# Kernel tuning notes

Hardware: AMD Instinct MI355X
Metric: run time of the kernel (lower is better)

## Reference

```python
import jax, jax.numpy as jnp
import numpy as np
import math

B, H, N, D = 4, 8, 2048, 64


def setup_inputs() -> dict:
    key = jax.random.key(0)
    kq, kk, kv = jax.random.split(key, 3)
    q = jax.random.normal(kq, (B, H, N, D), dtype=jnp.float32)
    k = jax.random.normal(kk, (B, H, N, D), dtype=jnp.float32)
    v = jax.random.normal(kv, (B, H, N, D), dtype=jnp.float32)
    return {"q": q, "k": k, "v": v}


def reference(q, k, v):
    # global_attention_Sub: expanded squared L2 distance ||q_i - k_j||^2
    # = qq_i - 2 q_i.k_j + kk_j, then softmax(-dist/sqrt(D)) @ v.
    scale = math.sqrt(q.shape[-1])
    inner = -2.0 * jnp.einsum('bhnd,bhmd->bhnm', q, k)          # [B,H,N,N]
    qq = jnp.sum(q * q, axis=-1, keepdims=True)                  # [B,H,N,1]
    kk = jnp.sum(k * k, axis=-1, keepdims=True)                  # [B,H,N,1]
    diff_sq = qq + inner + jnp.swapaxes(kk, -1, -2)              # [B,H,N,N]
    attn = jax.nn.softmax(-diff_sq / scale, axis=-1)
    x = jnp.einsum('bhnm,bhmd->bhnd', attn, v)                   # [B,H,N,D]
    return jnp.transpose(x, (0, 2, 1, 3))                        # [B,N,H,D]
```

## Files before the change

### kernel.cpp

```cpp
#include <hip/hip_runtime.h>

typedef __bf16 bf16x4 __attribute__((ext_vector_type(4)));
typedef __bf16 bf16x8 __attribute__((ext_vector_type(8)));
typedef float floatx4 __attribute__((ext_vector_type(4)));

constexpr int Bc = 4, Hc = 8, Nc = 2048, Dc = 64;
constexpr int BQ = 128;
constexpr int WQ = 32;
constexpr int TK = 64;
constexpr int NT = Nc / TK;
constexpr int SPS = 72;
constexpr float LOG2E = 1.44269504088896340736f;

constexpr size_t KSW_OFF = 0;
constexpr size_t VSW_OFF = (size_t)32 * NT * 8192;
constexpr size_t KKN_OFF = VSW_OFF * 2;

typedef __attribute__((address_space(1))) const unsigned int gu32;
typedef __attribute__((address_space(3))) unsigned int lu32;
__device__ __forceinline__ void dma16(const void* g, void* l) {
    __builtin_amdgcn_global_load_lds((gu32*)g, (lu32*)l, 16, 0, 0);
}
__device__ __forceinline__ void dma4(const void* g, void* l) {
    __builtin_amdgcn_global_load_lds((gu32*)g, (lu32*)l, 4, 0, 0);
}

__global__ __launch_bounds__(256) void prep_kernel(
    const float* __restrict__ Kg, const float* __restrict__ Vg, char* __restrict__ ws)
{
    __shared__ float sT[64 * 68];
    const int tid = threadIdx.x;
    const int jt = blockIdx.x, bh = blockIdx.y;

    __bf16* Ksw = (__bf16*)(ws + KSW_OFF) + ((size_t)bh * NT + jt) * 4096;
    __bf16* Vsw = (__bf16*)(ws + VSW_OFF) + ((size_t)bh * NT + jt) * 4096;
    float*  kkn = (float*)(ws + KKN_OFF) + (size_t)bh * Nc + jt * 64;
    const size_t tb = ((size_t)bh * Nc + jt * 64) * Dc;

#pragma unroll
    for (int cc = 0; cc < 2; ++cc) {
        const int g   = tid + cc * 256;
        const int key = g >> 3, kcx = g & 7;
        const int kc  = kcx ^ (key & 7);
        const float* src = Kg + tb + key * 64 + kc * 8;
        float4 a = *(const float4*)src;
        float4 b = *(const float4*)(src + 4);
        float ss = a.x*a.x + a.y*a.y + a.z*a.z + a.w*a.w
                 + b.x*b.x + b.y*b.y + b.z*b.z + b.w*b.w;
        ss += __shfl_xor(ss, 1);
        ss += __shfl_xor(ss, 2);
        ss += __shfl_xor(ss, 4);
        if (kcx == 0) kkn[key] = -(ss * 0.125f * LOG2E);
        bf16x8 c8;
        c8[0]=(__bf16)a.x; c8[1]=(__bf16)a.y; c8[2]=(__bf16)a.z; c8[3]=(__bf16)a.w;
        c8[4]=(__bf16)b.x; c8[5]=(__bf16)b.y; c8[6]=(__bf16)b.z; c8[7]=(__bf16)b.w;
        *(bf16x8*)(Ksw + g * 8) = c8;
    }

    {
        const int js = tid >> 2, dc = (tid & 3) * 16;
        const float* vr = Vg + tb + js * 64 + dc;
        float* dst = &sT[js * 68 + dc];
        *(float4*)dst       = *(const float4*)vr;
        *(float4*)(dst + 4) = *(const float4*)(vr + 4);
        *(float4*)(dst + 8) = *(const float4*)(vr + 8);
        *(float4*)(dst + 12)= *(const float4*)(vr + 12);
    }
    __syncthreads();

#pragma unroll
    for (int cc = 0; cc < 2; ++cc) {
        const int g = tid + cc * 256;
        const int d = g >> 3, kcx = g & 7;
        const int kc = kcx ^ (d & 7);
        bf16x8 c8;
#pragma unroll
        for (int e = 0; e < 8; ++e) {
            const int ee = (e + kcx) & 7;
            c8[ee] = (__bf16)sT[(kc * 8 + ee) * 68 + d];
        }
        *(bf16x8*)(Vsw + g * 8) = c8;
    }
}

__global__ __launch_bounds__(256, 2) void attn_kernel(
    const float* __restrict__ Qg, const char* __restrict__ ws, float* __restrict__ Og)
{
    __shared__ __align__(16) __bf16 sK[2][4096];
    __shared__ __align__(16) __bf16 sV[2][4096];
    __shared__ __align__(16) float  skk[2][64];
    __shared__ __align__(16) __bf16 sP[BQ * SPS];
    __shared__ __align__(16) float  sl[BQ];

    const int tid  = threadIdx.x;
    const int wave = tid >> 6;
    const int lane = tid & 63;
    const int qd   = lane >> 4;
    const int c    = lane & 15;

    const int qt = blockIdx.x;
    const int bh = blockIdx.y;

    const char* Kimg = ws + KSW_OFF + (size_t)bh * NT * 8192;
    const char* Vimg = ws + VSW_OFF + (size_t)bh * NT * 8192;
    const float* kkp = (const float*)(ws + KKN_OFF) + (size_t)bh * Nc;

    const float qscale = 0.25f * LOG2E;
    const int i0 = qt * BQ + wave * WQ;

    bf16x8 qf[2][2];
#pragma unroll
    for (int h = 0; h < 2; ++h) {
        const float* qrow = Qg + ((size_t)bh * Nc + i0 + h * 16 + c) * Dc + qd * 8;
#pragma unroll
        for (int ks = 0; ks < 2; ++ks) {
            float4 a = *(const float4*)(qrow + ks * 32);
            float4 b = *(const float4*)(qrow + ks * 32 + 4);
            bf16x8 f;
            f[0] = (__bf16)(a.x * qscale); f[1] = (__bf16)(a.y * qscale);
            f[2] = (__bf16)(a.z * qscale); f[3] = (__bf16)(a.w * qscale);
            f[4] = (__bf16)(b.x * qscale); f[5] = (__bf16)(b.y * qscale);
            f[6] = (__bf16)(b.z * qscale); f[7] = (__bf16)(b.w * qscale);
            qf[h][ks] = f;
        }
    }

    const int koff0 = c * 64 + ((qd ^ (c & 7)) << 3);
    const int koff1 = c * 64 + (((4 + qd) ^ (c & 7)) << 3);

    floatx4 oacc[2][4];
#pragma unroll
    for (int h = 0; h < 2; ++h)
#pragma unroll
        for (int dt = 0; dt < 4; ++dt)
#pragma unroll
            for (int e = 0; e < 4; ++e) oacc[h][dt][e] = 0.f;
    float lp[2] = {0.f, 0.f};

    auto stage = [&](int jt2, int b) {
        const char* ki = Kimg + (size_t)jt2 * 8192;
        const char* vi = Vimg + (size_t)jt2 * 8192;
#pragma unroll
        for (int i = 0; i < 2; ++i) {
            const int off    = wave * 2048 + i * 1024 + lane * 16;
            const int ldsoff = wave * 2048 + i * 1024;
            dma16(ki + off, (char*)&sK[b][0] + ldsoff);
            dma16(vi + off, (char*)&sV[b][0] + ldsoff);
        }
        if (wave == 3) dma4(kkp + jt2 * 64 + lane, &skk[b][0]);
    };

    stage(0, 0);

    for (int jt = 0; jt < NT; ++jt) {
        const int b = jt & 1;
        __syncthreads();
        if (jt + 1 < NT) stage(jt + 1, b ^ 1);

        floatx4 st[2][4];
#pragma unroll
        for (int kt = 0; kt < 4; ++kt) {
            floatx4 kkf = *(const floatx4*)&skk[b][kt * 16 + qd * 4];
            st[0][kt] = kkf; st[1][kt] = kkf;
        }
#pragma unroll
        for (int kt = 0; kt < 4; ++kt) {
            const __bf16* kbase = &sK[b][kt * 1024];
            bf16x8 kf0 = *(const bf16x8*)(kbase + koff0);
            bf16x8 kf1 = *(const bf16x8*)(kbase + koff1);
            st[0][kt] = __builtin_amdgcn_mfma_f32_16x16x32_bf16(kf0, qf[0][0], st[0][kt], 0, 0, 0);
            st[0][kt] = __builtin_amdgcn_mfma_f32_16x16x32_bf16(kf1, qf[0][1], st[0][kt], 0, 0, 0);
            st[1][kt] = __builtin_amdgcn_mfma_f32_16x16x32_bf16(kf0, qf[1][0], st[1][kt], 0, 0, 0);
            st[1][kt] = __builtin_amdgcn_mfma_f32_16x16x32_bf16(kf1, qf[1][1], st[1][kt], 0, 0, 0);
        }

#pragma unroll
        for (int h = 0; h < 2; ++h) {
            const int prow = wave * WQ + h * 16 + c;
#pragma unroll
            for (int kt = 0; kt < 4; ++kt) {
                float p0 = __builtin_amdgcn_exp2f(st[h][kt][0]);
                float p1 = __builtin_amdgcn_exp2f(st[h][kt][1]);
                float p2 = __builtin_amdgcn_exp2f(st[h][kt][2]);
                float p3 = __builtin_amdgcn_exp2f(st[h][kt][3]);
                lp[h] += (p0 + p1) + (p2 + p3);
                bf16x4 pk;
                pk[0] = (__bf16)p0; pk[1] = (__bf16)p1;
                pk[2] = (__bf16)p2; pk[3] = (__bf16)p3;
                *(bf16x4*)&sP[prow * SPS + kt * 16 + qd * 4] = pk;
            }
        }
        bf16x8 pf[2][2];
#pragma unroll
        for (int h = 0; h < 2; ++h)
#pragma unroll
            for (int ks = 0; ks < 2; ++ks)
                pf[h][ks] = *(const bf16x8*)&sP[(wave * WQ + h * 16 + c) * SPS + ks * 32 + qd * 8];

#pragma unroll
        for (int dt = 0; dt < 4; ++dt) {
            const __bf16* vbase = &sV[b][dt * 1024];
            bf16x8 vf0 = *(const bf16x8*)(vbase + koff0);
            bf16x8 vf1 = *(const bf16x8*)(vbase + koff1);
            oacc[0][dt] = __builtin_amdgcn_mfma_f32_16x16x32_bf16(pf[0][0], vf0, oacc[0][dt], 0, 0, 0);
            oacc[0][dt] = __builtin_amdgcn_mfma_f32_16x16x32_bf16(pf[0][1], vf1, oacc[0][dt], 0, 0, 0);
            oacc[1][dt] = __builtin_amdgcn_mfma_f32_16x16x32_bf16(pf[1][0], vf0, oacc[1][dt], 0, 0, 0);
            oacc[1][dt] = __builtin_amdgcn_mfma_f32_16x16x32_bf16(pf[1][1], vf1, oacc[1][dt], 0, 0, 0);
        }
    }

#pragma unroll
    for (int h = 0; h < 2; ++h) {
        float l = lp[h];
        l += __shfl_xor(l, 16);
        l += __shfl_xor(l, 32);
        if (qd == 0) sl[wave * WQ + h * 16 + c] = l;
    }
    const int b_ = bh >> 3, hh = bh & 7;
#pragma unroll
    for (int h = 0; h < 2; ++h) {
        floatx4 lf = *(const floatx4*)&sl[wave * WQ + h * 16 + qd * 4];
#pragma unroll
        for (int r = 0; r < 4; ++r) {
            const float inv = 1.f / lf[r];
            const int i = i0 + h * 16 + qd * 4 + r;
            float* orow = Og + (((size_t)b_ * Nc + i) * Hc + hh) * Dc + c;
#pragma unroll
            for (int dt = 0; dt < 4; ++dt)
                orow[dt * 16] = oacc[h][dt][r] * inv;
        }
    }
}

extern "C" void kernel_launch(void* const* d_in, const int* in_sizes, int n_in,
                              void* d_out, int out_size, void* d_ws, size_t ws_size,
                              hipStream_t stream) {
    const float* q = (const float*)d_in[0];
    const float* k = (const float*)d_in[1];
    const float* v = (const float*)d_in[2];
    float* out = (float*)d_out;
    char* ws = (char*)d_ws;
    prep_kernel<<<dim3(NT, Bc * Hc), 256, 0, stream>>>(k, v, ws);
    attn_kernel<<<dim3(Nc / BQ, Bc * Hc), 256, 0, stream>>>(q, ws, out);
}
```

Before: 140.8 us.

## Software-pipeline PV MMA one tile behind QK to overlap exp with MFMA

Restructures the attention loop so the P·V matrix multiply for the previous key tile runs right after the current tile's QK^T MFMAs, before the exp2 softmax step. This lets the exp/convert work overlap with independent MFMA work instead of being serialised. V staging moves to a triple buffer so the previous tile's V stays resident while the next one is loaded, and the final tile's PV is done after the loop. It costs extra LDS for the third V buffer and extra registers for the carried P fragments, which may lower occupancy.

Result: faster. 137.2 us (-2.5%).

```diff
diff --git a/kernel.cpp b/kernel.cpp
--- a/kernel.cpp
+++ b/kernel.cpp
@@ -56,7 +56,6 @@
         c8[4]=(__bf16)b.x; c8[5]=(__bf16)b.y; c8[6]=(__bf16)b.z; c8[7]=(__bf16)b.w;
         *(bf16x8*)(Ksw + g * 8) = c8;
     }
-
     {
         const int js = tid >> 2, dc = (tid & 3) * 16;
         const float* vr = Vg + tb + js * 64 + dc;
@@ -67,7 +66,6 @@
         *(float4*)(dst + 12)= *(const float4*)(vr + 12);
     }
     __syncthreads();
-
 #pragma unroll
     for (int cc = 0; cc < 2; ++cc) {
         const int g = tid + cc * 256;
@@ -87,7 +85,7 @@
     const float* __restrict__ Qg, const char* __restrict__ ws, float* __restrict__ Og)
 {
     __shared__ __align__(16) __bf16 sK[2][4096];
-    __shared__ __align__(16) __bf16 sV[2][4096];
+    __shared__ __align__(16) __bf16 sVall[3 * 4096];
     __shared__ __align__(16) float  skk[2][64];
     __shared__ __align__(16) __bf16 sP[BQ * SPS];
     __shared__ __align__(16) float  sl[BQ];
@@ -137,25 +135,31 @@
             for (int e = 0; e < 4; ++e) oacc[h][dt][e] = 0.f;
     float lp[2] = {0.f, 0.f};
 
-    auto stage = [&](int jt2, int b) {
+    __bf16* vprev = &sVall[2 * 4096];
+    __bf16* vcur  = &sVall[0];
+    __bf16* vnext = &sVall[1 * 4096];
+
+    auto stage = [&](int jt2, int kb, __bf16* vdst) {
         const char* ki = Kimg + (size_t)jt2 * 8192;
         const char* vi = Vimg + (size_t)jt2 * 8192;
 #pragma unroll
         for (int i = 0; i < 2; ++i) {
             const int off    = wave * 2048 + i * 1024 + lane * 16;
             const int ldsoff = wave * 2048 + i * 1024;
-            dma16(ki + off, (char*)&sK[b][0] + ldsoff);
-            dma16(vi + off, (char*)&sV[b][0] + ldsoff);
-        }
-        if (wave == 3) dma4(kkp + jt2 * 64 + lane, &skk[b][0]);
+            dma16(ki + off, (char*)&sK[kb][0] + ldsoff);
+            dma16(vi + off, (char*)vdst + ldsoff);
+        }
+        if (wave == 3) dma4(kkp + jt2 * 64 + lane, &skk[kb][0]);
     };
 
-    stage(0, 0);
+    stage(0, 0, vcur);
+
+    bf16x8 pfp[2][2];
 
     for (int jt = 0; jt < NT; ++jt) {
         const int b = jt & 1;
         __syncthreads();
-        if (jt + 1 < NT) stage(jt + 1, b ^ 1);
+        if (jt + 1 < NT) stage(jt + 1, b ^ 1, vnext);
 
         floatx4 st[2][4];
 #pragma unroll
@@ -172,6 +176,19 @@
             st[0][kt] = __builtin_amdgcn_mfma_f32_16x16x32_bf16(kf1, qf[0][1], st[0][kt], 0, 0, 0);
             st[1][kt] = __builtin_amdgcn_mfma_f32_16x16x32_bf16(kf0, qf[1][0], st[1][kt], 0, 0, 0);
             st[1][kt] = __builtin_amdgcn_mfma_f32_16x16x32_bf16(kf1, qf[1][1], st[1][kt], 0, 0, 0);
+        }
+
+        if (jt > 0) {
+#pragma unroll
+            for (int dt = 0; dt < 4; ++dt) {
+                const __bf16* vbase = vprev + dt * 1024;
+                bf16x8 vf0 = *(const bf16x8*)(vbase + koff0);
+                bf16x8 vf1 = *(const bf16x8*)(vbase + koff1);
+                oacc[0][dt] = __builtin_amdgcn_mfma_f32_16x16x32_bf16(pfp[0][0], vf0, oacc[0][dt], 0, 0, 0);
+                oacc[0][dt] = __builtin_amdgcn_mfma_f32_16x16x32_bf16(pfp[0][1], vf1, oacc[0][dt], 0, 0, 0);
+                oacc[1][dt] = __builtin_amdgcn_mfma_f32_16x16x32_bf16(pfp[1][0], vf0, oacc[1][dt], 0, 0, 0);
+                oacc[1][dt] = __builtin_amdgcn_mfma_f32_16x16x32_bf16(pfp[1][1], vf1, oacc[1][dt], 0, 0, 0);
+            }
         }
 
 #pragma unroll
@@ -190,23 +207,24 @@
                 *(bf16x4*)&sP[prow * SPS + kt * 16 + qd * 4] = pk;
             }
         }
-        bf16x8 pf[2][2];
 #pragma unroll
         for (int h = 0; h < 2; ++h)
 #pragma unroll
             for (int ks = 0; ks < 2; ++ks)
-                pf[h][ks] = *(const bf16x8*)&sP[(wave * WQ + h * 16 + c) * SPS + ks * 32 + qd * 8];
-
-#pragma unroll
-        for (int dt = 0; dt < 4; ++dt) {
-            const __bf16* vbase = &sV[b][dt * 1024];
-            bf16x8 vf0 = *(const bf16x8*)(vbase + koff0);
-            bf16x8 vf1 = *(const bf16x8*)(vbase + koff1);
-            oacc[0][dt] = __builtin_amdgcn_mfma_f32_16x16x32_bf16(pf[0][0], vf0, oacc[0][dt], 0, 0, 0);
-            oacc[0][dt] = __builtin_amdgcn_mfma_f32_16x16x32_bf16(pf[0][1], vf1, oacc[0][dt], 0, 0, 0);
-            oacc[1][dt] = __builtin_amdgcn_mfma_f32_16x16x32_bf16(pf[1][0], vf0, oacc[1][dt], 0, 0, 0);
-            oacc[1][dt] = __builtin_amdgcn_mfma_f32_16x16x32_bf16(pf[1][1], vf1, oacc[1][dt], 0, 0, 0);
-        }
+                pfp[h][ks] = *(const bf16x8*)&sP[(wave * WQ + h * 16 + c) * SPS + ks * 32 + qd * 8];
+
+        __bf16* t = vprev; vprev = vcur; vcur = vnext; vnext = t;
+    }
+
+#pragma unroll
+    for (int dt = 0; dt < 4; ++dt) {
+        const __bf16* vbase = vprev + dt * 1024;
+        bf16x8 vf0 = *(const bf16x8*)(vbase + koff0);
+        bf16x8 vf1 = *(const bf16x8*)(vbase + koff1);
+        oacc[0][dt] = __builtin_amdgcn_mfma_f32_16x16x32_bf16(pfp[0][0], vf0, oacc[0][dt], 0, 0, 0);
+        oacc[0][dt] = __builtin_amdgcn_mfma_f32_16x16x32_bf16(pfp[0][1], vf1, oacc[0][dt], 0, 0, 0);
+        oacc[1][dt] = __builtin_amdgcn_mfma_f32_16x16x32_bf16(pfp[1][0], vf0, oacc[1][dt], 0, 0, 0);
+        oacc[1][dt] = __builtin_amdgcn_mfma_f32_16x16x32_bf16(pfp[1][1], vf1, oacc[1][dt], 0, 0, 0);
     }
 
 #pragma unroll
```
